# Optimization experiments

Hardware: AMD Instinct MI355X
Metric: run time of the kernel (lower is better)

Reference implementation:

```python
import jax, jax.numpy as jnp
import numpy as np

# Standard NF4 codebook (QLoRA), sorted ascending, values in [-1, 1]
_NF4_CODE = np.array([
    -1.0, -0.6961928009986877, -0.5250730514526367, -0.39491748809814453,
    -0.28444138169288635, -0.18477343022823334, -0.09105003625154495, 0.0,
    0.07958029955625534, 0.16093020141124725, 0.24611230194568634,
    0.33791524171829224, 0.44070982933044434, 0.5626170039176941,
    0.7229568362236023, 1.0], dtype=np.float32)

BLOCK = 64           # NF4 block size (per-block absmax scale)
SCALE_BLOCK = 256    # double-quant: scales quantized to 8 bits per 256 scales


def nf4_quant_dequant(w):
    """Fake NF4 quantize->dequantize of weight [out, in] (QLoRA, block=64,
    8-bit double-quantized scales per 256 blocks)."""
    out_dim, in_dim = w.shape
    code = jnp.asarray(_NF4_CODE, dtype=w.dtype)
    wb = w.reshape(-1, BLOCK)                              # [nb, 64]
    absmax = jnp.max(jnp.abs(wb), axis=1)                  # [nb]
    # double quantization of scales: 8-bit symmetric per scale block
    sb = absmax.reshape(-1, SCALE_BLOCK)                   # [nsb, 256]
    s_amax = jnp.max(sb, axis=1, keepdims=True)
    s_amax = jnp.where(s_amax == 0, 1.0, s_amax)
    q8 = jnp.clip(jnp.round(sb / s_amax * 127.0), -127, 127)
    scale_dq = (q8 / 127.0 * s_amax).reshape(-1, 1)        # [nb, 1]
    # quantize normalized weights to nearest NF4 code (midpoint search)
    safe_absmax = jnp.where(absmax == 0, 1.0, absmax)[:, None]
    norm = wb / safe_absmax                                # in [-1, 1]
    boundaries = (code[:-1] + code[1:]) * 0.5              # [15]
    idx = jnp.searchsorted(boundaries, norm)               # nearest code index
    w_dq = code[idx] * scale_dq                            # dequantize
    return w_dq.reshape(out_dim, in_dim)


def setup_inputs() -> dict:
    key = jax.random.key(0)
    kx, kw = jax.random.split(key)
    x = jax.random.normal(kx, (16384, 4096), dtype=jnp.float32)
    weight = jax.random.normal(kw, (4096, 4096), dtype=jnp.float32) * 0.02
    return {"x": x, "weight": weight}


def reference(x, weight):
    # forward: F.linear(x, dequantize(nf4_quantize(weight)))
    w_dq = nf4_quant_dequant(weight)
    return x @ w_dq.T  # [tokens, out_dim]
```

## Files before the change

kernel.cpp:

```cpp
#include <hip/hip_runtime.h>
#include <stdint.h>


typedef __bf16 bf16x8 __attribute__((ext_vector_type(8)));
typedef float f32x4 __attribute__((ext_vector_type(4)));

constexpr float NF4_CODE[16] = {
    -1.0f, -0.6961928009986877f, -0.5250730514526367f, -0.39491748809814453f,
    -0.28444138169288635f, -0.18477343022823334f, -0.09105003625154495f, 0.0f,
    0.07958029955625534f, 0.16093020141124725f, 0.24611230194568634f,
    0.33791524171829224f, 0.44070982933044434f, 0.5626170039176941f,
    0.7229568362236023f, 1.0f};
constexpr float NF4_BND[15] = {
    0.5f * (NF4_CODE[0] + NF4_CODE[1]),   0.5f * (NF4_CODE[1] + NF4_CODE[2]),
    0.5f * (NF4_CODE[2] + NF4_CODE[3]),   0.5f * (NF4_CODE[3] + NF4_CODE[4]),
    0.5f * (NF4_CODE[4] + NF4_CODE[5]),   0.5f * (NF4_CODE[5] + NF4_CODE[6]),
    0.5f * (NF4_CODE[6] + NF4_CODE[7]),   0.5f * (NF4_CODE[7] + NF4_CODE[8]),
    0.5f * (NF4_CODE[8] + NF4_CODE[9]),   0.5f * (NF4_CODE[9] + NF4_CODE[10]),
    0.5f * (NF4_CODE[10] + NF4_CODE[11]), 0.5f * (NF4_CODE[11] + NF4_CODE[12]),
    0.5f * (NF4_CODE[12] + NF4_CODE[13]), 0.5f * (NF4_CODE[13] + NF4_CODE[14]),
    0.5f * (NF4_CODE[14] + NF4_CODE[15])};

__device__ __forceinline__ unsigned short f2bf(float f) {
  unsigned int u = __float_as_uint(f);
  u += 0x7fffu + ((u >> 16) & 1u);
  return (unsigned short)(u >> 16);
}

__global__ __launch_bounds__(256) void nf4_dequant(const float* __restrict__ w,
                                                   unsigned short* __restrict__ wdq) {
  __shared__ float s_am[256];
  __shared__ float s_code[16];
  const int t = threadIdx.x;
  if (t < 16) s_code[t] = NF4_CODE[t];

  const size_t base = (size_t)blockIdx.x * 16384 + (size_t)t * 64;
  const f32x4* src = (const f32x4*)(w + base);
  f32x4 v[16];
  float amax = 0.f;
#pragma unroll
  for (int i = 0; i < 16; ++i) {
    v[i] = __builtin_nontemporal_load(src + i);
    amax = fmaxf(amax, fmaxf(fmaxf(fabsf(v[i][0]), fabsf(v[i][1])),
                             fmaxf(fabsf(v[i][2]), fabsf(v[i][3]))));
  }
  s_am[t] = amax;
  __syncthreads();
#pragma unroll
  for (int off = 128; off > 0; off >>= 1) {
    if (t < off) s_am[t] = fmaxf(s_am[t], s_am[t + off]);
    __syncthreads();
  }
  const float s_amax = s_am[0];
  const float sa = (s_amax == 0.f) ? 1.f : s_amax;
  float q8 = rintf(amax / sa * 127.f);
  q8 = fminf(fmaxf(q8, -127.f), 127.f);
  const float scale = (q8 / 127.f) * sa;
  const float safe_am = (amax == 0.f) ? 1.f : amax;

  auto dq1 = [&](float x) -> unsigned short {
    const float norm = x / safe_am;
    int idx = 0;
#pragma unroll
    for (int j = 0; j < 15; ++j) idx += (NF4_BND[j] < norm) ? 1 : 0;
    return f2bf(s_code[idx] * scale);
  };

  uint4* dst = (uint4*)(wdq + base);
#pragma unroll
  for (int i = 0; i < 8; ++i) {
    const f32x4 a = v[2 * i], b = v[2 * i + 1];
    uint4 o;
    o.x = (unsigned)dq1(a[0]) | ((unsigned)dq1(a[1]) << 16);
    o.y = (unsigned)dq1(a[2]) | ((unsigned)dq1(a[3]) << 16);
    o.z = (unsigned)dq1(b[0]) | ((unsigned)dq1(b[1]) << 16);
    o.w = (unsigned)dq1(b[2]) | ((unsigned)dq1(b[3]) << 16);
    dst[i] = o;
  }
}

__global__ __launch_bounds__(256) void cast_f32_to_bf16(const float* __restrict__ x,
                                                        unsigned short* __restrict__ y,
                                                        size_t n8) {
  const size_t stride = (size_t)gridDim.x * 256;
  for (size_t i = (size_t)blockIdx.x * 256 + threadIdx.x; i < n8; i += stride) {
    const f32x4* s = (const f32x4*)x + i * 2;
    const f32x4 a = __builtin_nontemporal_load(s);
    const f32x4 b = __builtin_nontemporal_load(s + 1);
    uint4 o;
    o.x = (unsigned)f2bf(a[0]) | ((unsigned)f2bf(a[1]) << 16);
    o.y = (unsigned)f2bf(a[2]) | ((unsigned)f2bf(a[3]) << 16);
    o.z = (unsigned)f2bf(b[0]) | ((unsigned)f2bf(b[1]) << 16);
    o.w = (unsigned)f2bf(b[2]) | ((unsigned)f2bf(b[3]) << 16);
    ((uint4*)y)[i] = o;
  }
}


__device__ __forceinline__ void gld16(const unsigned short* g, unsigned short* l) {
  __builtin_amdgcn_global_load_lds(
      (__attribute__((address_space(1))) void*)g,
      (__attribute__((address_space(3))) void*)l, 16, 0, 0);
}

#define BAR __builtin_amdgcn_s_barrier()
#define LGKM0 asm volatile("s_waitcnt lgkmcnt(0)" ::: "memory")
#define VMW(n) asm volatile("s_waitcnt vmcnt(" #n ")" ::: "memory")

#define STG(buf, ab, hf, ks)                                                   \
  do {                                                                         \
    const unsigned short* g_ =                                                 \
        ((ab) ? gB0 : gA0) + (size_t)(hf)*HOFF + (size_t)(ks);                 \
    unsigned short* l_ =                                                       \
        lds + (buf)*32768 + (ab)*16384 + (hf)*8192 + wvoff;                    \
    gld16(g_, l_);                                                             \
    gld16(g_ + 64 * (size_t)K, l_ + 4096);                                     \
  } while (0)

#define RD_A(buf, mh)                                                          \
  do {                                                                         \
    _Pragma("unroll") for (int i4 = 0; i4 < 4; ++i4) {                         \
      afr[i4][0] = *(const bf16x8*)(pa + (buf)*32768 + (mh)*4096 +             \
                                    i4 * 1024 + aoff0);                        \
      afr[i4][1] = *(const bf16x8*)(pa + (buf)*32768 + (mh)*4096 +             \
                                    i4 * 1024 + aoff1);                        \
    }                                                                          \
  } while (0)

#define RD_B(buf, nh)                                                          \
  do {                                                                         \
    _Pragma("unroll") for (int j2 = 0; j2 < 2; ++j2) {                         \
      bfr[(nh)*2 + j2][0] = *(const bf16x8*)(pb + (buf)*32768 + (nh)*2048 +    \
                                             j2 * 1024 + aoff0);               \
      bfr[(nh)*2 + j2][1] = *(const bf16x8*)(pb + (buf)*32768 + (nh)*2048 +    \
                                             j2 * 1024 + aoff1);               \
    }                                                                          \
  } while (0)

#define MM(mh, nh)                                                             \
  do {                                                                         \
    __builtin_amdgcn_s_setprio(1);                                             \
    _Pragma("unroll") for (int ks = 0; ks < 2; ++ks) {                         \
      _Pragma("unroll") for (int i4 = 0; i4 < 4; ++i4) {                       \
        _Pragma("unroll") for (int j2 = 0; j2 < 2; ++j2) {                     \
          acc[(mh)*4 + i4][(nh)*2 + j2] =                                      \
              __builtin_amdgcn_mfma_f32_16x16x32_bf16(                         \
                  afr[i4][ks], bfr[(nh)*2 + j2][ks],                           \
                  acc[(mh)*4 + i4][(nh)*2 + j2], 0, 0, 0);                     \
        }                                                                      \
      }                                                                        \
    }                                                                          \
    __builtin_amdgcn_s_setprio(0);                                             \
  } while (0)

__global__ __launch_bounds__(512, 2) void gemm8p(const unsigned short* __restrict__ A,
                                                 const unsigned short* __restrict__ Bt,
                                                 float* __restrict__ C,
                                                 int M, int N, int K) {
  __shared__ __align__(16) unsigned short lds[65536];

  const int t = threadIdx.x;
  const int wave = t >> 6;
  const int lane = t & 63;

  const int nbx = N >> 8;
  const int nwg = nbx * (M >> 8);
  const int q8 = nwg >> 3, r8 = nwg & 7;
  const int xcd = (int)blockIdx.x & 7, off = (int)blockIdx.x >> 3;
  const int wg =
      (xcd < r8 ? xcd * (q8 + 1) : r8 * (q8 + 1) + (xcd - r8) * q8) + off;
  const int bm = (wg / nbx) << 8;
  const int bn = (wg % nbx) << 8;

  const size_t HOFF = (size_t)128 * K;
  const int srow = wave * 8 + (lane >> 3);
  const int sj = (lane & 7) ^ (lane >> 3);
  const unsigned short* gA0 = A + (size_t)(bm + srow) * K + sj * 8;
  const unsigned short* gB0 = Bt + (size_t)(bn + srow) * K + sj * 8;
  const int wvoff = wave * 512;

  const int wm = wave >> 2;
  const int wn = wave & 3;
  const int quad = lane >> 4;
  const int lrow = lane & 15;
  const int s0 = quad ^ (lrow & 7);
  const int aoff0 = lrow * 64 + s0 * 8;
  const int aoff1 = lrow * 64 + (s0 ^ 4) * 8;
  const unsigned short* pa = lds + wm * 8192;
  const unsigned short* pb = lds + 16384 + (wn >> 1) * 8192 + (wn & 1) * 4096;

  f32x4 acc[8][4];
  const f32x4 zero = {0.f, 0.f, 0.f, 0.f};
#pragma unroll
  for (int i = 0; i < 8; ++i)
#pragma unroll
    for (int j = 0; j < 4; ++j) acc[i][j] = zero;

  bf16x8 afr[4][2];
  bf16x8 bfr[4][2];

  STG(0, 0, 0, 0);
  STG(0, 1, 0, 0);
  STG(0, 1, 1, 0);
  STG(0, 0, 1, 0);
  STG(1, 1, 0, 64);
  STG(1, 0, 0, 64);
  STG(1, 1, 1, 64);
  VMW(6);
  BAR;

  const int niter = K >> 7;
  for (int it = 0; it < niter; ++it) {
    const int kt = it << 7;
    const int kA = kt + 64;
    int kB0 = kt + 128; if (kB0 > K - 64) kB0 = K - 64;
    int kB1 = kt + 192; if (kB1 > K - 64) kB1 = K - 64;

    RD_A(0, 0); RD_B(0, 0); STG(1, 0, 1, kA);
    BAR; LGKM0; MM(0, 0); BAR;
    RD_B(0, 1); STG(0, 1, 0, kB0);
    BAR; LGKM0; MM(0, 1); BAR;
    RD_A(0, 1); STG(0, 0, 0, kB0);
    BAR; LGKM0; MM(1, 0); BAR;
    STG(0, 1, 1, kB0); VMW(6);
    BAR; MM(1, 1); BAR;
    RD_A(1, 0); RD_B(1, 0); STG(0, 0, 1, kB0);
    BAR; LGKM0; MM(0, 0); BAR;
    RD_B(1, 1); STG(1, 1, 0, kB1);
    BAR; LGKM0; MM(0, 1); BAR;
    RD_A(1, 1); STG(1, 0, 0, kB1);
    BAR; LGKM0; MM(1, 0); BAR;
    STG(1, 1, 1, kB1); VMW(6);
    BAR; MM(1, 1); BAR;
  }

  VMW(0);

  const int crow = bm + wm * 128 + quad * 4;
  const int ccol = bn + wn * 64 + lrow;
#pragma unroll
  for (int i = 0; i < 8; ++i) {
#pragma unroll
    for (int j = 0; j < 4; ++j) {
      float* cp = C + (size_t)(crow + i * 16) * N + (ccol + j * 16);
#pragma unroll
      for (int r = 0; r < 4; ++r)
        __builtin_nontemporal_store(acc[i][j][r], cp + (size_t)r * N);
    }
  }
}

extern "C" void kernel_launch(void* const* d_in, const int* in_sizes, int n_in,
                              void* d_out, int out_size, void* d_ws, size_t ws_size,
                              hipStream_t stream) {
  const float* x = (const float*)d_in[0];
  const float* w = (const float*)d_in[1];
  const int K = 4096;
  const int M = in_sizes[0] / K;
  const int N = in_sizes[1] / K;

  unsigned short* wdq = (unsigned short*)d_ws;
  unsigned short* xbf = wdq + (size_t)in_sizes[1];

  nf4_dequant<<<in_sizes[1] / 16384, 256, 0, stream>>>(w, wdq);
  cast_f32_to_bf16<<<4096, 256, 0, stream>>>(x, xbf, (size_t)in_sizes[0] / 8);
  dim3 grid((N / 256) * (M / 256));
  gemm8p<<<grid, 512, 0, stream>>>(xbf, wdq, (float*)d_out, M, N, K);
}
```

Before: 887.5 us.

## Interleave LDS fragment reads with MFMA and rework NF4 dequant reduction

The GEMM main loop is rescheduled so that LDS fragment reads for the next sub-tile are issued between the two k-halves of the current MFMA group. Explicit lgkmcnt waits are removed and global-to-LDS stages are grouped in pairs behind vmcnt waits. The goal is to hide LDS read latency behind matrix-core work and cut barrier stalls, at the cost of a more fragile ordering of reads, writes and barriers that relies on the compiler inserting correct waits. The NF4 dequant kernel also switches to coalesced strided loads with wave-shuffle reductions instead of an LDS tree reduction.

```diff
diff --git a/kernel.cpp b/kernel.cpp
--- a/kernel.cpp
+++ b/kernel.cpp
@@ -30,52 +30,58 @@
 __global__ __launch_bounds__(256) void nf4_dequant(const float* __restrict__ w,
                                                    unsigned short* __restrict__ wdq) {
   __shared__ float s_am[256];
+  __shared__ float s_red[4];
   __shared__ float s_code[16];
   const int t = threadIdx.x;
   if (t < 16) s_code[t] = NF4_CODE[t];
-
-  const size_t base = (size_t)blockIdx.x * 16384 + (size_t)t * 64;
+  const size_t base = (size_t)blockIdx.x * 16384;
   const f32x4* src = (const f32x4*)(w + base);
+
   f32x4 v[16];
-  float amax = 0.f;
-#pragma unroll
-  for (int i = 0; i < 16; ++i) {
-    v[i] = __builtin_nontemporal_load(src + i);
-    amax = fmaxf(amax, fmaxf(fmaxf(fabsf(v[i][0]), fabsf(v[i][1])),
-                             fmaxf(fabsf(v[i][2]), fabsf(v[i][3]))));
-  }
-  s_am[t] = amax;
+#pragma unroll
+  for (int k = 0; k < 16; ++k) {
+    v[k] = __builtin_nontemporal_load(src + k * 256 + t);
+    float m = fmaxf(fmaxf(fabsf(v[k][0]), fabsf(v[k][1])),
+                    fmaxf(fabsf(v[k][2]), fabsf(v[k][3])));
+    m = fmaxf(m, __shfl_xor(m, 1));
+    m = fmaxf(m, __shfl_xor(m, 2));
+    m = fmaxf(m, __shfl_xor(m, 4));
+    m = fmaxf(m, __shfl_xor(m, 8));
+    if ((t & 15) == 0) s_am[k * 16 + (t >> 4)] = m;
+  }
   __syncthreads();
-#pragma unroll
-  for (int off = 128; off > 0; off >>= 1) {
-    if (t < off) s_am[t] = fmaxf(s_am[t], s_am[t + off]);
-    __syncthreads();
-  }
-  const float s_amax = s_am[0];
+  float m = s_am[t];
+  m = fmaxf(m, __shfl_xor(m, 1));
+  m = fmaxf(m, __shfl_xor(m, 2));
+  m = fmaxf(m, __shfl_xor(m, 4));
+  m = fmaxf(m, __shfl_xor(m, 8));
+  m = fmaxf(m, __shfl_xor(m, 16));
+  m = fmaxf(m, __shfl_xor(m, 32));
+  if ((t & 63) == 0) s_red[t >> 6] = m;
+  __syncthreads();
+  const float s_amax = fmaxf(fmaxf(s_red[0], s_red[1]), fmaxf(s_red[2], s_red[3]));
   const float sa = (s_amax == 0.f) ? 1.f : s_amax;
-  float q8 = rintf(amax / sa * 127.f);
-  q8 = fminf(fmaxf(q8, -127.f), 127.f);
-  const float scale = (q8 / 127.f) * sa;
-  const float safe_am = (amax == 0.f) ? 1.f : amax;
-
-  auto dq1 = [&](float x) -> unsigned short {
-    const float norm = x / safe_am;
-    int idx = 0;
-#pragma unroll
-    for (int j = 0; j < 15; ++j) idx += (NF4_BND[j] < norm) ? 1 : 0;
-    return f2bf(s_code[idx] * scale);
-  };
-
-  uint4* dst = (uint4*)(wdq + base);
-#pragma unroll
-  for (int i = 0; i < 8; ++i) {
-    const f32x4 a = v[2 * i], b = v[2 * i + 1];
-    uint4 o;
-    o.x = (unsigned)dq1(a[0]) | ((unsigned)dq1(a[1]) << 16);
-    o.y = (unsigned)dq1(a[2]) | ((unsigned)dq1(a[3]) << 16);
-    o.z = (unsigned)dq1(b[0]) | ((unsigned)dq1(b[1]) << 16);
-    o.w = (unsigned)dq1(b[2]) | ((unsigned)dq1(b[3]) << 16);
-    dst[i] = o;
+
+#pragma unroll
+  for (int k = 0; k < 16; ++k) {
+    const float am = s_am[k * 16 + (t >> 4)];
+    float q8 = rintf(am / sa * 127.f);
+    q8 = fminf(fmaxf(q8, -127.f), 127.f);
+    const float scale = (q8 / 127.f) * sa;
+    const float safe_am = (am == 0.f) ? 1.f : am;
+    unsigned r[4];
+#pragma unroll
+    for (int e = 0; e < 4; ++e) {
+      const float norm = v[k][e] / safe_am;
+      int idx = 0;
+#pragma unroll
+      for (int j = 0; j < 15; ++j) idx += (NF4_BND[j] < norm) ? 1 : 0;
+      r[e] = (unsigned)f2bf(s_code[idx] * scale);
+    }
+    uint2 o;
+    o.x = r[0] | (r[1] << 16);
+    o.y = r[2] | (r[3] << 16);
+    ((uint2*)(wdq + base))[k * 256 + t] = o;
   }
 }
 
@@ -103,9 +109,15 @@
       (__attribute__((address_space(3))) void*)l, 16, 0, 0);
 }
 
-#define BAR __builtin_amdgcn_s_barrier()
-#define LGKM0 asm volatile("s_waitcnt lgkmcnt(0)" ::: "memory")
+#define BARX                                                                   \
+  do {                                                                         \
+    asm volatile("" ::: "memory");                                             \
+    __builtin_amdgcn_s_barrier();                                              \
+    asm volatile("" ::: "memory");                                             \
+  } while (0)
 #define VMW(n) asm volatile("s_waitcnt vmcnt(" #n ")" ::: "memory")
+#define SP1 __builtin_amdgcn_s_setprio(1)
+#define SP0 __builtin_amdgcn_s_setprio(0)
 
 #define STG(buf, ab, hf, ks)                                                   \
   do {                                                                         \
@@ -117,40 +129,33 @@
     gld16(g_ + 64 * (size_t)K, l_ + 4096);                                     \
   } while (0)
 
-#define RD_A(buf, mh)                                                          \
+#define RDA(buf, mh, ks)                                                       \
   do {                                                                         \
     _Pragma("unroll") for (int i4 = 0; i4 < 4; ++i4) {                         \
-      afr[i4][0] = *(const bf16x8*)(pa + (buf)*32768 + (mh)*4096 +             \
-                                    i4 * 1024 + aoff0);                        \
-      afr[i4][1] = *(const bf16x8*)(pa + (buf)*32768 + (mh)*4096 +             \
-                                    i4 * 1024 + aoff1);                        \
+      afr[i4][ks] = *(const bf16x8*)(pa + (buf)*32768 + (mh)*4096 +            \
+                                     i4 * 1024 + ((ks) ? aoff1 : aoff0));      \
     }                                                                          \
   } while (0)
 
-#define RD_B(buf, nh)                                                          \
+#define RDB(buf, nh, ks)                                                       \
   do {                                                                         \
     _Pragma("unroll") for (int j2 = 0; j2 < 2; ++j2) {                         \
-      bfr[(nh)*2 + j2][0] = *(const bf16x8*)(pb + (buf)*32768 + (nh)*2048 +    \
-                                             j2 * 1024 + aoff0);               \
-      bfr[(nh)*2 + j2][1] = *(const bf16x8*)(pb + (buf)*32768 + (nh)*2048 +    \
-                                             j2 * 1024 + aoff1);               \
+      bfr[(nh)*2 + j2][ks] = *(const bf16x8*)(pb + (buf)*32768 + (nh)*2048 +   \
+                                              j2 * 1024 +                      \
+                                              ((ks) ? aoff1 : aoff0));         \
     }                                                                          \
   } while (0)
 
-#define MM(mh, nh)                                                             \
-  do {                                                                         \
-    __builtin_amdgcn_s_setprio(1);                                             \
-    _Pragma("unroll") for (int ks = 0; ks < 2; ++ks) {                         \
-      _Pragma("unroll") for (int i4 = 0; i4 < 4; ++i4) {                       \
-        _Pragma("unroll") for (int j2 = 0; j2 < 2; ++j2) {                     \
-          acc[(mh)*4 + i4][(nh)*2 + j2] =                                      \
-              __builtin_amdgcn_mfma_f32_16x16x32_bf16(                         \
-                  afr[i4][ks], bfr[(nh)*2 + j2][ks],                           \
-                  acc[(mh)*4 + i4][(nh)*2 + j2], 0, 0, 0);                     \
-        }                                                                      \
+#define MMH(mh, nh, ks)                                                        \
+  do {                                                                         \
+    _Pragma("unroll") for (int i4 = 0; i4 < 4; ++i4) {                         \
+      _Pragma("unroll") for (int j2 = 0; j2 < 2; ++j2) {                       \
+        acc[(mh)*4 + i4][(nh)*2 + j2] =                                        \
+            __builtin_amdgcn_mfma_f32_16x16x32_bf16(                           \
+                afr[i4][ks], bfr[(nh)*2 + j2][ks],                             \
+                acc[(mh)*4 + i4][(nh)*2 + j2], 0, 0, 0);                       \
       }                                                                        \
     }                                                                          \
-    __builtin_amdgcn_s_setprio(0);                                             \
   } while (0)
 
 __global__ __launch_bounds__(512, 2) void gemm8p(const unsigned short* __restrict__ A,
@@ -199,39 +204,37 @@
   bf16x8 afr[4][2];
   bf16x8 bfr[4][2];
 
-  STG(0, 0, 0, 0);
-  STG(0, 1, 0, 0);
-  STG(0, 1, 1, 0);
-  STG(0, 0, 1, 0);
-  STG(1, 1, 0, 64);
-  STG(1, 0, 0, 64);
-  STG(1, 1, 1, 64);
-  VMW(6);
-  BAR;
+  STG(0, 1, 0, 0); STG(0, 1, 1, 0);
+  STG(0, 0, 0, 0); STG(0, 0, 1, 0);
+  STG(1, 1, 0, 64); STG(1, 1, 1, 64);
+  STG(1, 0, 0, 64); STG(1, 0, 1, 64);
+  VMW(8);
+  BARX;
+  RDA(0, 0, 0); RDA(0, 0, 1);
+  RDB(0, 0, 0); RDB(0, 0, 1);
 
   const int niter = K >> 7;
   for (int it = 0; it < niter; ++it) {
     const int kt = it << 7;
-    const int kA = kt + 64;
-    int kB0 = kt + 128; if (kB0 > K - 64) kB0 = K - 64;
-    int kB1 = kt + 192; if (kB1 > K - 64) kB1 = K - 64;
-
-    RD_A(0, 0); RD_B(0, 0); STG(1, 0, 1, kA);
-    BAR; LGKM0; MM(0, 0); BAR;
-    RD_B(0, 1); STG(0, 1, 0, kB0);
-    BAR; LGKM0; MM(0, 1); BAR;
-    RD_A(0, 1); STG(0, 0, 0, kB0);
-    BAR; LGKM0; MM(1, 0); BAR;
-    STG(0, 1, 1, kB0); VMW(6);
-    BAR; MM(1, 1); BAR;
-    RD_A(1, 0); RD_B(1, 0); STG(0, 0, 1, kB0);
-    BAR; LGKM0; MM(0, 0); BAR;
-    RD_B(1, 1); STG(1, 1, 0, kB1);
-    BAR; LGKM0; MM(0, 1); BAR;
-    RD_A(1, 1); STG(1, 0, 0, kB1);
-    BAR; LGKM0; MM(1, 0); BAR;
-    STG(1, 1, 1, kB1); VMW(6);
-    BAR; MM(1, 1); BAR;
+    int kc2 = kt + 128; if (kc2 > K - 64) kc2 = K - 64;
+    int kc3 = kt + 192; if (kc3 > K - 64) kc3 = K - 64;
+
+    VMW(8); BARX;
+    SP1; MMH(0, 0, 0); RDB(0, 1, 0); MMH(0, 0, 1); RDB(0, 1, 1); SP0;
+    VMW(8); STG(0, 1, 0, kc2); STG(0, 1, 1, kc2); BARX;
+    SP1; MMH(0, 1, 0); RDA(0, 1, 0); MMH(0, 1, 1); RDA(0, 1, 1); SP0;
+    VMW(8); STG(0, 0, 0, kc2); STG(0, 0, 1, kc2); BARX;
+    SP1; MMH(1, 0, 0); RDB(1, 0, 0); MMH(1, 0, 1); RDB(1, 0, 1); SP0;
+    VMW(8); BARX;
+    SP1; MMH(1, 1, 0); RDA(1, 0, 0); MMH(1, 1, 1); RDA(1, 0, 1); SP0;
+    VMW(8); BARX;
+    SP1; MMH(0, 0, 0); RDB(1, 1, 0); MMH(0, 0, 1); RDB(1, 1, 1); SP0;
+    VMW(8); STG(1, 1, 0, kc3); STG(1, 1, 1, kc3); BARX;
+    SP1; MMH(0, 1, 0); RDA(1, 1, 0); MMH(0, 1, 1); RDA(1, 1, 1); SP0;
+    VMW(8); STG(1, 0, 0, kc3); STG(1, 0, 1, kc3); BARX;
+    SP1; MMH(1, 0, 0); RDB(0, 0, 0); MMH(1, 0, 1); RDB(0, 0, 1); SP0;
+    VMW(8); BARX;
+    SP1; MMH(1, 1, 0); RDA(0, 0, 0); MMH(1, 1, 1); RDA(0, 0, 1); SP0;
   }
 
   VMW(0);
```

Result: faster. 863.8 us (-2.7%).
